# Kernel tuning notes

Hardware: AMD Instinct MI355X
Metric: run time of the kernel (lower is better)

## Reference

```python
import jax, jax.numpy as jnp
import numpy as np

INPUT_SIZE = 32
HIDDEN = 128
OUT_SIZE = 1
B, S = 256, 1200


def _gru_layer(x_seq, W_ih, W_hh, b_ih, b_hh):
    """PyTorch-convention GRU layer. x_seq: [B,S,D] -> [B,S,H].
    W_ih: [3H,D], W_hh: [3H,H], gate order (r,z,n)."""
    Bsz = x_seq.shape[0]
    H = W_hh.shape[1]
    # Precompute input projections for all timesteps (one big GEMM).
    gates_x = jnp.einsum('bsd,gd->bsg', x_seq, W_ih) + b_ih  # [B,S,3H]

    def step(h, gx):
        gh = h @ W_hh.T + b_hh                 # [B,3H]
        xr, xz, xn = jnp.split(gx, 3, axis=-1)
        hr, hz, hn = jnp.split(gh, 3, axis=-1)
        r = jax.nn.sigmoid(xr + hr)
        z = jax.nn.sigmoid(xz + hz)
        n = jnp.tanh(xn + r * hn)
        h_new = (1.0 - z) * n + z * h
        return h_new, h_new

    h0 = jnp.zeros((Bsz, H), x_seq.dtype)
    _, ys = jax.lax.scan(step, h0, jnp.swapaxes(gates_x, 0, 1))  # [S,B,H]
    return jnp.swapaxes(ys, 0, 1)


def setup_inputs() -> dict:
    key = jax.random.key(0)
    ks = jax.random.split(key, 12)
    s_in = 1.0 / np.sqrt(HIDDEN)  # PyTorch GRU init scale
    d = {
        'x': jax.random.normal(ks[0], (B, S, INPUT_SIZE), dtype=jnp.float32),
        'W_ih0': jax.random.uniform(ks[1], (3 * HIDDEN, INPUT_SIZE), jnp.float32, -s_in, s_in),
        'W_hh0': jax.random.uniform(ks[2], (3 * HIDDEN, HIDDEN), jnp.float32, -s_in, s_in),
        'b_ih0': jax.random.uniform(ks[3], (3 * HIDDEN,), jnp.float32, -s_in, s_in),
        'b_hh0': jax.random.uniform(ks[4], (3 * HIDDEN,), jnp.float32, -s_in, s_in),
        'W_ih1': jax.random.uniform(ks[5], (3 * HIDDEN, HIDDEN), jnp.float32, -s_in, s_in),
        'W_hh1': jax.random.uniform(ks[6], (3 * HIDDEN, HIDDEN), jnp.float32, -s_in, s_in),
        'b_ih1': jax.random.uniform(ks[7], (3 * HIDDEN,), jnp.float32, -s_in, s_in),
        'b_hh1': jax.random.uniform(ks[8], (3 * HIDDEN,), jnp.float32, -s_in, s_in),
        'W_lin': jax.random.uniform(ks[9], (OUT_SIZE, HIDDEN), jnp.float32, -s_in, s_in),
        'b_lin': jax.random.uniform(ks[10], (OUT_SIZE,), jnp.float32, -s_in, s_in),
    }
    return d


def reference(x, W_ih0, W_hh0, b_ih0, b_hh0, W_ih1, W_hh1, b_ih1, b_hh1, W_lin, b_lin):
    h1 = _gru_layer(x, W_ih0, W_hh0, b_ih0, b_hh0)   # [B,S,H]  (dropout inactive at eval)
    h2 = _gru_layer(h1, W_ih1, W_hh1, b_ih1, b_hh1)  # [B,S,H]
    out = jax.nn.relu(h2)
    out = jnp.einsum('bsh,oh->bso', out, W_lin) + b_lin  # [B,S,OUT_SIZE]
    return out.reshape(-1, 12)
```

## Files before the change

kernel.cpp:

```cpp
#include <hip/hip_runtime.h>
#include <hip/hip_bf16.h>


typedef _Float16 h2 __attribute__((ext_vector_type(2)));

#if __has_builtin(__builtin_amdgcn_fdot2)
__device__ __forceinline__ float dot2f(h2 a, h2 b, float c) {
  return __builtin_amdgcn_fdot2(a, b, c, false);
}
#else
__device__ __forceinline__ float dot2f(h2 a, h2 b, float c) {
  return c + (float)a[0] * (float)b[0] + (float)a[1] * (float)b[1];
}
#endif

__device__ __forceinline__ h2 pack2(float x, float y) {
  h2 r; r[0] = (_Float16)x; r[1] = (_Float16)y; return r;
}
__device__ __forceinline__ float sigm(float x) {
  return 1.0f / (1.0f + __expf(-x));
}
__device__ __forceinline__ float tanh_f(float x) {
  x = fminf(fmaxf(x, -15.f), 15.f);
  float e = __expf(2.f * x);
  return (e - 1.f) / (e + 1.f);
}
__device__ __forceinline__ float hsum(float4 v) { return (v.x + v.y) + (v.z + v.w); }

__device__ __forceinline__ void load_pack8(const float* p, h2* w) {
  float4 a = ((const float4*)p)[0], b = ((const float4*)p)[1];
  w[0] = pack2(a.x, a.y); w[1] = pack2(a.z, a.w);
  w[2] = pack2(b.x, b.y); w[3] = pack2(b.z, b.w);
}

#define SEQ 1200
#define HID 128
#define INSZ 32

#define DOT4Q(W, F, ACC)                                                \
  ACC = dot2f((W)[0], __builtin_bit_cast(h2, (F).x), ACC);              \
  ACC = dot2f((W)[1], __builtin_bit_cast(h2, (F).y), ACC);              \
  ACC = dot2f((W)[2], __builtin_bit_cast(h2, (F).z), ACC);              \
  ACC = dot2f((W)[3], __builtin_bit_cast(h2, (F).w), ACC);

#define DOT16Q(W, FA, FB, FC, FD, ACC)                                  \
  DOT4Q(&(W)[0],  FA, ACC) DOT4Q(&(W)[4],  FB, ACC)                     \
  DOT4Q(&(W)[8],  FC, ACC) DOT4Q(&(W)[12], FD, ACC)

__global__ __launch_bounds__(512, 2) void gru_fused(
    const float* __restrict__ x,
    const float* __restrict__ Wih0, const float* __restrict__ Whh0,
    const float* __restrict__ bih0, const float* __restrict__ bhh0,
    const float* __restrict__ Wih1, const float* __restrict__ Whh1,
    const float* __restrict__ bih1, const float* __restrict__ bhh1,
    const float* __restrict__ Wlin, const float* __restrict__ blin,
    float* __restrict__ out)
{
  const int tid = threadIdx.x;
  const int b   = blockIdx.x;
  const int q   = tid >> 2;
  const int ql  = tid & 3;

  __shared__ float G1p[4 * 512];
  __shared__ float G2p[4 * 512];
  __shared__ float  s0f[HID], s1f[HID];
  __shared__ float4 s0h4[16], s1h4[16];
  __shared__ float4 xh[2][4];
  __shared__ float  pbf[32];

  h2 wi0[3][4];
  h2 wh0[3][16];
  h2 wi1[3][16];
  h2 wh1[3][16];
#pragma unroll
  for (int rr = 0; rr < 3; ++rr) {
    const int row = rr * HID + q;
    load_pack8(Wih0 + (size_t)row * INSZ + ql * 8, wi0[rr]);
#pragma unroll
    for (int c = 0; c < 4; ++c) {
      load_pack8(Whh0 + (size_t)row * HID + ql * 32 + c * 8, &wh0[rr][c * 4]);
      load_pack8(Wih1 + (size_t)row * HID + ql * 32 + c * 8, &wi1[rr][c * 4]);
      load_pack8(Whh1 + (size_t)row * HID + ql * 32 + c * 8, &wh1[rr][c * 4]);
    }
  }

  float bA = 0.f, bB = 0.f, bC = 0.f, bD = 0.f, wl = 0.f;
  if (tid < 128) {
    bA = bih1[tid] + bhh1[tid];
    bB = bih1[HID + tid] + bhh1[HID + tid];
    bC = bih1[2 * HID + tid];
    bD = bhh1[2 * HID + tid];
    wl = Wlin[tid];
  } else if (tid < 256) {
    const int i = tid - 128;
    bA = bih0[i] + bhh0[i];
    bB = bih0[HID + i] + bhh0[HID + i];
    bC = bih0[2 * HID + i];
    bD = bhh0[2 * HID + i];
  }
  const float blv = blin[0];

  if (tid < HID) { s0f[tid] = 0.f; s1f[tid] = 0.f; }
  if (tid < 64) { ((float*)s0h4)[tid] = 0.f; ((float*)s1h4)[tid] = 0.f; }
  const float2* xsrc = (const float2*)x + (size_t)b * SEQ * (INSZ / 2);
  if (tid < 16) {
    float2 v = xsrc[tid];
    ((h2*)xh[0])[tid] = pack2(v.x, v.y);
  }
  __syncthreads();

  float* outp = out + (size_t)b * SEQ;

  for (int t = -1; t < SEQ; ++t) {
    {
      const int buf = (t + 1) & 1;
      const float4 xq = xh[buf][ql];
      const float4 sA = s0h4[ql * 4 + 0], sB = s0h4[ql * 4 + 1],
                   sC = s0h4[ql * 4 + 2], sD = s0h4[ql * 4 + 3];
      const float4 tA = s1h4[ql * 4 + 0], tB = s1h4[ql * 4 + 1],
                   tC = s1h4[ql * 4 + 2], tD = s1h4[ql * 4 + 3];
      float a0 = 0.f, a1 = 0.f, a2 = 0.f, a3 = 0.f;
      DOT4Q(wi0[0], xq, a0) DOT16Q(wh0[0], sA, sB, sC, sD, a0)
      DOT4Q(wi0[1], xq, a1) DOT16Q(wh0[1], sA, sB, sC, sD, a1)
      DOT4Q(wi0[2], xq, a2)
      DOT16Q(wh0[2], sA, sB, sC, sD, a3)
      float c0 = 0.f, c1 = 0.f, c2 = 0.f, c3 = 0.f;
      DOT16Q(wi1[0], sA, sB, sC, sD, c0) DOT16Q(wh1[0], tA, tB, tC, tD, c0)
      DOT16Q(wi1[1], sA, sB, sC, sD, c1) DOT16Q(wh1[1], tA, tB, tC, tD, c1)
      DOT16Q(wi1[2], sA, sB, sC, sD, c2)
      DOT16Q(wh1[2], tA, tB, tC, tD, c3)
      G1p[tid] = a0; G1p[512 + tid] = a1; G1p[1024 + tid] = a2; G1p[1536 + tid] = a3;
      G2p[tid] = c0; G2p[512 + tid] = c1; G2p[1024 + tid] = c2; G2p[1536 + tid] = c3;
    }
    float2 xn;
    if ((tid & ~15) == 256) {
      const int ti = (t + 2 < SEQ) ? t + 2 : SEQ - 1;
      xn = xsrc[(size_t)ti * 16 + (tid - 256)];
    }
    __syncthreads();

    if (tid < 128) {
      if (t >= 0) {
        const float4* G4 = (const float4*)G2p;
        float4 r4 = G4[tid], z4 = G4[128 + tid], x4 = G4[256 + tid], h4 = G4[384 + tid];
        float r = sigm(hsum(r4) + bA);
        float z = sigm(hsum(z4) + bB);
        float n = tanh_f(hsum(x4) + bC + r * (hsum(h4) + bD));
        float h = (1.f - z) * n + z * s1f[tid];
        s1f[tid] = h;
        ((_Float16*)s1h4)[tid] = (_Float16)h;
        float p = fmaxf(h, 0.f) * wl;
        p += __shfl_xor(p, 1, 64);
        p += __shfl_xor(p, 2, 64);
        p += __shfl_xor(p, 4, 64);
        if ((tid & 7) == 0) pbf[(t & 1) * 16 + (tid >> 3)] = p;
      }
    } else if (tid < 256) {
      const int i = tid - 128;
      const float4* G4 = (const float4*)G1p;
      float4 r4 = G4[i], z4 = G4[128 + i], x4 = G4[256 + i], h4 = G4[384 + i];
      float r = sigm(hsum(r4) + bA);
      float z = sigm(hsum(z4) + bB);
      float n = tanh_f(hsum(x4) + bC + r * (hsum(h4) + bD));
      float h = (1.f - z) * n + z * s0f[i];
      s0f[i] = h;
      ((_Float16*)s0h4)[i] = (_Float16)h;
    } else if (tid < 272) {
      ((h2*)xh[t & 1])[tid - 256] = pack2(xn.x, xn.y);
    } else if (tid == 320 && t >= 1) {
      const float4* p4 = (const float4*)(pbf + ((t - 1) & 1) * 16);
      outp[t - 1] = hsum(p4[0]) + hsum(p4[1]) + hsum(p4[2]) + hsum(p4[3]) + blv;
    }
    __syncthreads();
  }

  if (tid == 0) {
    const float4* p4 = (const float4*)(pbf + ((SEQ - 1) & 1) * 16);
    outp[SEQ - 1] = hsum(p4[0]) + hsum(p4[1]) + hsum(p4[2]) + hsum(p4[3]) + blv;
  }
}

extern "C" void kernel_launch(void* const* d_in, const int* in_sizes, int n_in,
                              void* d_out, int out_size, void* d_ws, size_t ws_size,
                              hipStream_t stream) {
  const float* x    = (const float*)d_in[0];
  const float* Wih0 = (const float*)d_in[1];
  const float* Whh0 = (const float*)d_in[2];
  const float* bih0 = (const float*)d_in[3];
  const float* bhh0 = (const float*)d_in[4];
  const float* Wih1 = (const float*)d_in[5];
  const float* Whh1 = (const float*)d_in[6];
  const float* bih1 = (const float*)d_in[7];
  const float* bhh1 = (const float*)d_in[8];
  const float* Wlin = (const float*)d_in[9];
  const float* blin = (const float*)d_in[10];
  float* outp = (float*)d_out;

  const int Bn = in_sizes[0] / (SEQ * INSZ);
  hipLaunchKernelGGL(gru_fused, dim3(Bn), dim3(512), 0, stream,
                     x, Wih0, Whh0, bih0, bhh0,
                     Wih1, Whh1, bih1, bhh1, Wlin, blin, outp);
}
```

Before: 1.354 ms.

## Split each gate-row dot product across eight threads with 1024-thread blocks

Doubles the block to 1024 threads so each gate row's dot products are split across 8 lanes instead of 4. Each thread now holds half as many packed fp16 weights in registers and does half the dot2 work per step, shortening the serial per-step critical path. In exchange, the gate-update threads must sum twice as many partials from shared memory, and barriers now span 16 waves. With 256 blocks, each CU likely holds only one block instead of possibly two.

```diff
diff --git a/kernel.cpp b/kernel.cpp
--- a/kernel.cpp
+++ b/kernel.cpp
@@ -43,11 +43,10 @@
   ACC = dot2f((W)[2], __builtin_bit_cast(h2, (F).z), ACC);              \
   ACC = dot2f((W)[3], __builtin_bit_cast(h2, (F).w), ACC);
 
-#define DOT16Q(W, FA, FB, FC, FD, ACC)                                  \
-  DOT4Q(&(W)[0],  FA, ACC) DOT4Q(&(W)[4],  FB, ACC)                     \
-  DOT4Q(&(W)[8],  FC, ACC) DOT4Q(&(W)[12], FD, ACC)
-
-__global__ __launch_bounds__(512, 2) void gru_fused(
+#define DOT8(W, FA, FB, ACC)                                            \
+  DOT4Q(&(W)[0], FA, ACC) DOT4Q(&(W)[4], FB, ACC)
+
+__global__ __launch_bounds__(1024) void gru_fused(
     const float* __restrict__ x,
     const float* __restrict__ Wih0, const float* __restrict__ Whh0,
     const float* __restrict__ bih0, const float* __restrict__ bhh0,
@@ -58,29 +57,30 @@
 {
   const int tid = threadIdx.x;
   const int b   = blockIdx.x;
-  const int q   = tid >> 2;
-  const int ql  = tid & 3;
-
-  __shared__ float G1p[4 * 512];
-  __shared__ float G2p[4 * 512];
+  const int oct = tid >> 3;
+  const int ko  = tid & 7;
+
+  __shared__ float G1p[4 * 1024];
+  __shared__ float G2p[4 * 1024];
   __shared__ float  s0f[HID], s1f[HID];
   __shared__ float4 s0h4[16], s1h4[16];
   __shared__ float4 xh[2][4];
   __shared__ float  pbf[32];
 
-  h2 wi0[3][4];
-  h2 wh0[3][16];
-  h2 wi1[3][16];
-  h2 wh1[3][16];
+  h2 wi0[3][2];
+  h2 wh0[3][8];
+  h2 wi1[3][8];
+  h2 wh1[3][8];
 #pragma unroll
   for (int rr = 0; rr < 3; ++rr) {
-    const int row = rr * HID + q;
-    load_pack8(Wih0 + (size_t)row * INSZ + ql * 8, wi0[rr]);
+    const int row = rr * HID + oct;
+    float4 v = *(const float4*)(Wih0 + (size_t)row * INSZ + ko * 4);
+    wi0[rr][0] = pack2(v.x, v.y); wi0[rr][1] = pack2(v.z, v.w);
 #pragma unroll
-    for (int c = 0; c < 4; ++c) {
-      load_pack8(Whh0 + (size_t)row * HID + ql * 32 + c * 8, &wh0[rr][c * 4]);
-      load_pack8(Wih1 + (size_t)row * HID + ql * 32 + c * 8, &wi1[rr][c * 4]);
-      load_pack8(Whh1 + (size_t)row * HID + ql * 32 + c * 8, &wh1[rr][c * 4]);
+    for (int c = 0; c < 2; ++c) {
+      load_pack8(Whh0 + (size_t)row * HID + ko * 16 + c * 8, &wh0[rr][c * 4]);
+      load_pack8(Wih1 + (size_t)row * HID + ko * 16 + c * 8, &wi1[rr][c * 4]);
+      load_pack8(Whh1 + (size_t)row * HID + ko * 16 + c * 8, &wh1[rr][c * 4]);
     }
   }
 
@@ -114,23 +114,25 @@
   for (int t = -1; t < SEQ; ++t) {
     {
       const int buf = (t + 1) & 1;
-      const float4 xq = xh[buf][ql];
-      const float4 sA = s0h4[ql * 4 + 0], sB = s0h4[ql * 4 + 1],
-                   sC = s0h4[ql * 4 + 2], sD = s0h4[ql * 4 + 3];
-      const float4 tA = s1h4[ql * 4 + 0], tB = s1h4[ql * 4 + 1],
-                   tC = s1h4[ql * 4 + 2], tD = s1h4[ql * 4 + 3];
+      const float2 xq = ((const float2*)xh[buf])[ko];
+      const h2 x0 = __builtin_bit_cast(h2, xq.x);
+      const h2 x1 = __builtin_bit_cast(h2, xq.y);
+      const float4 sA = s0h4[ko * 2], sB = s0h4[ko * 2 + 1];
+      const float4 tA = s1h4[ko * 2], tB = s1h4[ko * 2 + 1];
       float a0 = 0.f, a1 = 0.f, a2 = 0.f, a3 = 0.f;
-      DOT4Q(wi0[0], xq, a0) DOT16Q(wh0[0], sA, sB, sC, sD, a0)
-      DOT4Q(wi0[1], xq, a1) DOT16Q(wh0[1], sA, sB, sC, sD, a1)
-      DOT4Q(wi0[2], xq, a2)
-      DOT16Q(wh0[2], sA, sB, sC, sD, a3)
+      a0 = dot2f(wi0[0][0], x0, a0); a0 = dot2f(wi0[0][1], x1, a0);
+      DOT8(wh0[0], sA, sB, a0)
+      a1 = dot2f(wi0[1][0], x0, a1); a1 = dot2f(wi0[1][1], x1, a1);
+      DOT8(wh0[1], sA, sB, a1)
+      a2 = dot2f(wi0[2][0], x0, a2); a2 = dot2f(wi0[2][1], x1, a2);
+      DOT8(wh0[2], sA, sB, a3)
       float c0 = 0.f, c1 = 0.f, c2 = 0.f, c3 = 0.f;
-      DOT16Q(wi1[0], sA, sB, sC, sD, c0) DOT16Q(wh1[0], tA, tB, tC, tD, c0)
-      DOT16Q(wi1[1], sA, sB, sC, sD, c1) DOT16Q(wh1[1], tA, tB, tC, tD, c1)
-      DOT16Q(wi1[2], sA, sB, sC, sD, c2)
-      DOT16Q(wh1[2], tA, tB, tC, tD, c3)
-      G1p[tid] = a0; G1p[512 + tid] = a1; G1p[1024 + tid] = a2; G1p[1536 + tid] = a3;
-      G2p[tid] = c0; G2p[512 + tid] = c1; G2p[1024 + tid] = c2; G2p[1536 + tid] = c3;
+      DOT8(wi1[0], sA, sB, c0) DOT8(wh1[0], tA, tB, c0)
+      DOT8(wi1[1], sA, sB, c1) DOT8(wh1[1], tA, tB, c1)
+      DOT8(wi1[2], sA, sB, c2)
+      DOT8(wh1[2], tA, tB, c3)
+      G1p[tid] = a0; G1p[1024 + tid] = a1; G1p[2048 + tid] = a2; G1p[3072 + tid] = a3;
+      G2p[tid] = c0; G2p[1024 + tid] = c1; G2p[2048 + tid] = c2; G2p[3072 + tid] = c3;
     }
     float2 xn;
     if ((tid & ~15) == 256) {
@@ -142,10 +144,13 @@
     if (tid < 128) {
       if (t >= 0) {
         const float4* G4 = (const float4*)G2p;
-        float4 r4 = G4[tid], z4 = G4[128 + tid], x4 = G4[256 + tid], h4 = G4[384 + tid];
-        float r = sigm(hsum(r4) + bA);
-        float z = sigm(hsum(z4) + bB);
-        float n = tanh_f(hsum(x4) + bC + r * (hsum(h4) + bD));
+        float ra = hsum(G4[2 * tid])       + hsum(G4[2 * tid + 1]);
+        float za = hsum(G4[256 + 2 * tid]) + hsum(G4[257 + 2 * tid]);
+        float xa = hsum(G4[512 + 2 * tid]) + hsum(G4[513 + 2 * tid]);
+        float ha = hsum(G4[768 + 2 * tid]) + hsum(G4[769 + 2 * tid]);
+        float r = sigm(ra + bA);
+        float z = sigm(za + bB);
+        float n = tanh_f(xa + bC + r * (ha + bD));
         float h = (1.f - z) * n + z * s1f[tid];
         s1f[tid] = h;
         ((_Float16*)s1h4)[tid] = (_Float16)h;
@@ -158,10 +163,13 @@
     } else if (tid < 256) {
       const int i = tid - 128;
       const float4* G4 = (const float4*)G1p;
-      float4 r4 = G4[i], z4 = G4[128 + i], x4 = G4[256 + i], h4 = G4[384 + i];
-      float r = sigm(hsum(r4) + bA);
-      float z = sigm(hsum(z4) + bB);
-      float n = tanh_f(hsum(x4) + bC + r * (hsum(h4) + bD));
+      float ra = hsum(G4[2 * i])       + hsum(G4[2 * i + 1]);
+      float za = hsum(G4[256 + 2 * i]) + hsum(G4[257 + 2 * i]);
+      float xa = hsum(G4[512 + 2 * i]) + hsum(G4[513 + 2 * i]);
+      float ha = hsum(G4[768 + 2 * i]) + hsum(G4[769 + 2 * i]);
+      float r = sigm(ra + bA);
+      float z = sigm(za + bB);
+      float n = tanh_f(xa + bC + r * (ha + bD));
       float h = (1.f - z) * n + z * s0f[i];
       s0f[i] = h;
       ((_Float16*)s0h4)[i] = (_Float16)h;
@@ -197,7 +205,7 @@
   float* outp = (float*)d_out;
 
   const int Bn = in_sizes[0] / (SEQ * INSZ);
-  hipLaunchKernelGGL(gru_fused, dim3(Bn), dim3(512), 0, stream,
+  hipLaunchKernelGGL(gru_fused, dim3(Bn), dim3(1024), 0, stream,
                      x, Wih0, Whh0, bih0, bhh0,
                      Wih1, Whh1, bih1, bhh1, Wlin, blin, outp);
 }
```

After: 1.447 ms. 6.9% more time.

## Compute GRU gate matvecs with MFMA 16x16x32 f16 instead of fdot2

Applied to the files above, without the earlier changes.

Replaces the per-thread fdot2 matrix-vector products with MFMA instructions. Weights stay in registers as f16x8 A-fragments and the hidden state is broadcast as the B operand, so only column 0 of each 16x16 output is useful. Each wave covers 32 r/z rows and 16 n rows and writes the gate pre-activations to shared memory from lanes with lr==0. This removes the four-way partial-sum reduction and cuts instruction count per step, but wastes most of the MFMA output width and drops launch bounds to one block per CU.

```diff
diff --git a/kernel.cpp b/kernel.cpp
--- a/kernel.cpp
+++ b/kernel.cpp
@@ -2,21 +2,13 @@
 #include <hip/hip_bf16.h>
 
 
-typedef _Float16 h2 __attribute__((ext_vector_type(2)));
-
-#if __has_builtin(__builtin_amdgcn_fdot2)
-__device__ __forceinline__ float dot2f(h2 a, h2 b, float c) {
-  return __builtin_amdgcn_fdot2(a, b, c, false);
-}
-#else
-__device__ __forceinline__ float dot2f(h2 a, h2 b, float c) {
-  return c + (float)a[0] * (float)b[0] + (float)a[1] * (float)b[1];
-}
-#endif
-
-__device__ __forceinline__ h2 pack2(float x, float y) {
-  h2 r; r[0] = (_Float16)x; r[1] = (_Float16)y; return r;
-}
+typedef _Float16 f16x8 __attribute__((ext_vector_type(8)));
+typedef float f32x4 __attribute__((ext_vector_type(4)));
+
+#define SEQ 1200
+#define HID 128
+#define INSZ 32
+
 __device__ __forceinline__ float sigm(float x) {
   return 1.0f / (1.0f + __expf(-x));
 }
@@ -25,29 +17,18 @@
   float e = __expf(2.f * x);
   return (e - 1.f) / (e + 1.f);
 }
-__device__ __forceinline__ float hsum(float4 v) { return (v.x + v.y) + (v.z + v.w); }
-
-__device__ __forceinline__ void load_pack8(const float* p, h2* w) {
-  float4 a = ((const float4*)p)[0], b = ((const float4*)p)[1];
-  w[0] = pack2(a.x, a.y); w[1] = pack2(a.z, a.w);
-  w[2] = pack2(b.x, b.y); w[3] = pack2(b.z, b.w);
-}
-
-#define SEQ 1200
-#define HID 128
-#define INSZ 32
-
-#define DOT4Q(W, F, ACC)                                                \
-  ACC = dot2f((W)[0], __builtin_bit_cast(h2, (F).x), ACC);              \
-  ACC = dot2f((W)[1], __builtin_bit_cast(h2, (F).y), ACC);              \
-  ACC = dot2f((W)[2], __builtin_bit_cast(h2, (F).z), ACC);              \
-  ACC = dot2f((W)[3], __builtin_bit_cast(h2, (F).w), ACC);
-
-#define DOT16Q(W, FA, FB, FC, FD, ACC)                                  \
-  DOT4Q(&(W)[0],  FA, ACC) DOT4Q(&(W)[4],  FB, ACC)                     \
-  DOT4Q(&(W)[8],  FC, ACC) DOT4Q(&(W)[12], FD, ACC)
-
-__global__ __launch_bounds__(512, 2) void gru_fused(
+
+__device__ __forceinline__ f16x8 loadA(const float* p) {
+  float4 u = ((const float4*)p)[0], v = ((const float4*)p)[1];
+  f16x8 r;
+  r[0] = (_Float16)u.x; r[1] = (_Float16)u.y; r[2] = (_Float16)u.z; r[3] = (_Float16)u.w;
+  r[4] = (_Float16)v.x; r[5] = (_Float16)v.y; r[6] = (_Float16)v.z; r[7] = (_Float16)v.w;
+  return r;
+}
+
+#define MFMA(A, B, C) __builtin_amdgcn_mfma_f32_16x16x32_f16((A), (B), (C), 0, 0, 0)
+
+__global__ __launch_bounds__(512, 1) void gru_fused(
     const float* __restrict__ x,
     const float* __restrict__ Wih0, const float* __restrict__ Whh0,
     const float* __restrict__ bih0, const float* __restrict__ bhh0,
@@ -56,31 +37,42 @@
     const float* __restrict__ Wlin, const float* __restrict__ blin,
     float* __restrict__ out)
 {
-  const int tid = threadIdx.x;
-  const int b   = blockIdx.x;
-  const int q   = tid >> 2;
-  const int ql  = tid & 3;
-
-  __shared__ float G1p[4 * 512];
-  __shared__ float G2p[4 * 512];
-  __shared__ float  s0f[HID], s1f[HID];
-  __shared__ float4 s0h4[16], s1h4[16];
-  __shared__ float4 xh[2][4];
-  __shared__ float  pbf[32];
-
-  h2 wi0[3][4];
-  h2 wh0[3][16];
-  h2 wi1[3][16];
-  h2 wh1[3][16];
+  const int tid  = threadIdx.x;
+  const int b    = blockIdx.x;
+  const int wid  = tid >> 6;
+  const int lane = tid & 63;
+  const int lr   = lane & 15;
+  const int lg   = lane >> 4;
+
+  __shared__ float G1x[384], G1h[384];
+  __shared__ float G2x[384], G2h[384];
+  __shared__ float s0f[HID], s1f[HID];
+  __shared__ __align__(16) _Float16 s0h[HID], s1h[HID];
+  __shared__ __align__(16) _Float16 xh[2][INSZ];
+  __shared__ float pbf[32];
+
+  const int RZ0 = wid * 32, RZ1 = wid * 32 + 16, NR = 256 + wid * 16;
+
+  f16x8 Ax0, Ax1, AxN;
+  f16x8 Ah0[3][4], Ai1[3][4], Ah1w[3][4];
+  {
+    const int r0 = RZ0 + lr, r1 = RZ1 + lr, rn = NR + lr;
+    const int kb = lg * 8;
+    Ax0 = loadA(Wih0 + (size_t)r0 * INSZ + kb);
+    Ax1 = loadA(Wih0 + (size_t)r1 * INSZ + kb);
+    AxN = loadA(Wih0 + (size_t)rn * INSZ + kb);
 #pragma unroll
-  for (int rr = 0; rr < 3; ++rr) {
-    const int row = rr * HID + q;
-    load_pack8(Wih0 + (size_t)row * INSZ + ql * 8, wi0[rr]);
-#pragma unroll
-    for (int c = 0; c < 4; ++c) {
-      load_pack8(Whh0 + (size_t)row * HID + ql * 32 + c * 8, &wh0[rr][c * 4]);
-      load_pack8(Wih1 + (size_t)row * HID + ql * 32 + c * 8, &wi1[rr][c * 4]);
-      load_pack8(Whh1 + (size_t)row * HID + ql * 32 + c * 8, &wh1[rr][c * 4]);
+    for (int kt = 0; kt < 4; ++kt) {
+      const int ko = kt * 32 + kb;
+      Ah0[0][kt]  = loadA(Whh0 + (size_t)r0 * HID + ko);
+      Ah0[1][kt]  = loadA(Whh0 + (size_t)r1 * HID + ko);
+      Ah0[2][kt]  = loadA(Whh0 + (size_t)rn * HID + ko);
+      Ai1[0][kt]  = loadA(Wih1 + (size_t)r0 * HID + ko);
+      Ai1[1][kt]  = loadA(Wih1 + (size_t)r1 * HID + ko);
+      Ai1[2][kt]  = loadA(Wih1 + (size_t)rn * HID + ko);
+      Ah1w[0][kt] = loadA(Whh1 + (size_t)r0 * HID + ko);
+      Ah1w[1][kt] = loadA(Whh1 + (size_t)r1 * HID + ko);
+      Ah1w[2][kt] = loadA(Whh1 + (size_t)rn * HID + ko);
     }
   }
 
@@ -100,12 +92,14 @@
   }
   const float blv = blin[0];
 
-  if (tid < HID) { s0f[tid] = 0.f; s1f[tid] = 0.f; }
-  if (tid < 64) { ((float*)s0h4)[tid] = 0.f; ((float*)s1h4)[tid] = 0.f; }
+  if (tid < HID) {
+    s0f[tid] = 0.f; s1f[tid] = 0.f;
+    s0h[tid] = (_Float16)0.f; s1h[tid] = (_Float16)0.f;
+  }
   const float2* xsrc = (const float2*)x + (size_t)b * SEQ * (INSZ / 2);
   if (tid < 16) {
     float2 v = xsrc[tid];
-    ((h2*)xh[0])[tid] = pack2(v.x, v.y);
+    xh[0][2 * tid] = (_Float16)v.x; xh[0][2 * tid + 1] = (_Float16)v.y;
   }
   __syncthreads();
 
@@ -113,24 +107,43 @@
 
   for (int t = -1; t < SEQ; ++t) {
     {
-      const int buf = (t + 1) & 1;
-      const float4 xq = xh[buf][ql];
-      const float4 sA = s0h4[ql * 4 + 0], sB = s0h4[ql * 4 + 1],
-                   sC = s0h4[ql * 4 + 2], sD = s0h4[ql * 4 + 3];
-      const float4 tA = s1h4[ql * 4 + 0], tB = s1h4[ql * 4 + 1],
-                   tC = s1h4[ql * 4 + 2], tD = s1h4[ql * 4 + 3];
-      float a0 = 0.f, a1 = 0.f, a2 = 0.f, a3 = 0.f;
-      DOT4Q(wi0[0], xq, a0) DOT16Q(wh0[0], sA, sB, sC, sD, a0)
-      DOT4Q(wi0[1], xq, a1) DOT16Q(wh0[1], sA, sB, sC, sD, a1)
-      DOT4Q(wi0[2], xq, a2)
-      DOT16Q(wh0[2], sA, sB, sC, sD, a3)
-      float c0 = 0.f, c1 = 0.f, c2 = 0.f, c3 = 0.f;
-      DOT16Q(wi1[0], sA, sB, sC, sD, c0) DOT16Q(wh1[0], tA, tB, tC, tD, c0)
-      DOT16Q(wi1[1], sA, sB, sC, sD, c1) DOT16Q(wh1[1], tA, tB, tC, tD, c1)
-      DOT16Q(wi1[2], sA, sB, sC, sD, c2)
-      DOT16Q(wh1[2], tA, tB, tC, tD, c3)
-      G1p[tid] = a0; G1p[512 + tid] = a1; G1p[1024 + tid] = a2; G1p[1536 + tid] = a3;
-      G2p[tid] = c0; G2p[512 + tid] = c1; G2p[1024 + tid] = c2; G2p[1536 + tid] = c3;
+      f16x8 Bh1[4], Bh2[4], Bx;
+#pragma unroll
+      for (int kt = 0; kt < 4; ++kt) {
+        Bh1[kt] = *(const f16x8*)(s0h + kt * 32 + lg * 8);
+        Bh2[kt] = *(const f16x8*)(s1h + kt * 32 + lg * 8);
+      }
+      Bx = *(const f16x8*)(xh[(t + 1) & 1] + lg * 8);
+
+      const f32x4 Z = {0.f, 0.f, 0.f, 0.f};
+      f32x4 a0x = MFMA(Ax0, Bx, Z);
+      f32x4 a1x = MFMA(Ax1, Bx, Z);
+      f32x4 anx = MFMA(AxN, Bx, Z);
+      f32x4 a0h = Z, a1h = Z, anh = Z;
+      f32x4 c0x = Z, c1x = Z, cnx = Z, c0h = Z, c1h = Z, cnh = Z;
+#pragma unroll
+      for (int kt = 0; kt < 4; ++kt) {
+        a0h = MFMA(Ah0[0][kt],  Bh1[kt], a0h);
+        a1h = MFMA(Ah0[1][kt],  Bh1[kt], a1h);
+        anh = MFMA(Ah0[2][kt],  Bh1[kt], anh);
+        c0x = MFMA(Ai1[0][kt],  Bh1[kt], c0x);
+        c1x = MFMA(Ai1[1][kt],  Bh1[kt], c1x);
+        cnx = MFMA(Ai1[2][kt],  Bh1[kt], cnx);
+        c0h = MFMA(Ah1w[0][kt], Bh2[kt], c0h);
+        c1h = MFMA(Ah1w[1][kt], Bh2[kt], c1h);
+        cnh = MFMA(Ah1w[2][kt], Bh2[kt], cnh);
+      }
+      if (lr == 0) {
+        const int ro = lg * 4;
+        *(f32x4*)(G1x + RZ0 + ro) = a0x; *(f32x4*)(G1x + RZ1 + ro) = a1x;
+        *(f32x4*)(G1x + NR  + ro) = anx;
+        *(f32x4*)(G1h + RZ0 + ro) = a0h; *(f32x4*)(G1h + RZ1 + ro) = a1h;
+        *(f32x4*)(G1h + NR  + ro) = anh;
+        *(f32x4*)(G2x + RZ0 + ro) = c0x; *(f32x4*)(G2x + RZ1 + ro) = c1x;
+        *(f32x4*)(G2x + NR  + ro) = cnx;
+        *(f32x4*)(G2h + RZ0 + ro) = c0h; *(f32x4*)(G2h + RZ1 + ro) = c1h;
+        *(f32x4*)(G2h + NR  + ro) = cnh;
+      }
     }
     float2 xn;
     if ((tid & ~15) == 256) {
@@ -141,14 +154,12 @@
 
     if (tid < 128) {
       if (t >= 0) {
-        const float4* G4 = (const float4*)G2p;
-        float4 r4 = G4[tid], z4 = G4[128 + tid], x4 = G4[256 + tid], h4 = G4[384 + tid];
-        float r = sigm(hsum(r4) + bA);
-        float z = sigm(hsum(z4) + bB);
-        float n = tanh_f(hsum(x4) + bC + r * (hsum(h4) + bD));
+        float r = sigm(G2x[tid] + G2h[tid] + bA);
+        float z = sigm(G2x[HID + tid] + G2h[HID + tid] + bB);
+        float n = tanh_f(G2x[2 * HID + tid] + bC + r * (G2h[2 * HID + tid] + bD));
         float h = (1.f - z) * n + z * s1f[tid];
         s1f[tid] = h;
-        ((_Float16*)s1h4)[tid] = (_Float16)h;
+        s1h[tid] = (_Float16)h;
         float p = fmaxf(h, 0.f) * wl;
         p += __shfl_xor(p, 1, 64);
         p += __shfl_xor(p, 2, 64);
@@ -157,26 +168,29 @@
       }
     } else if (tid < 256) {
       const int i = tid - 128;
-      const float4* G4 = (const float4*)G1p;
-      float4 r4 = G4[i], z4 = G4[128 + i], x4 = G4[256 + i], h4 = G4[384 + i];
-      float r = sigm(hsum(r4) + bA);
-      float z = sigm(hsum(z4) + bB);
-      float n = tanh_f(hsum(x4) + bC + r * (hsum(h4) + bD));
+      float r = sigm(G1x[i] + G1h[i] + bA);
+      float z = sigm(G1x[HID + i] + G1h[HID + i] + bB);
+      float n = tanh_f(G1x[2 * HID + i] + bC + r * (G1h[2 * HID + i] + bD));
       float h = (1.f - z) * n + z * s0f[i];
       s0f[i] = h;
-      ((_Float16*)s0h4)[i] = (_Float16)h;
+      s0h[i] = (_Float16)h;
     } else if (tid < 272) {
-      ((h2*)xh[t & 1])[tid - 256] = pack2(xn.x, xn.y);
+      const int i = tid - 256;
+      xh[t & 1][2 * i] = (_Float16)xn.x; xh[t & 1][2 * i + 1] = (_Float16)xn.y;
     } else if (tid == 320 && t >= 1) {
       const float4* p4 = (const float4*)(pbf + ((t - 1) & 1) * 16);
-      outp[t - 1] = hsum(p4[0]) + hsum(p4[1]) + hsum(p4[2]) + hsum(p4[3]) + blv;
+      float4 u = p4[0], v = p4[1], w = p4[2], s = p4[3];
+      outp[t - 1] = (u.x + u.y + u.z + u.w) + (v.x + v.y + v.z + v.w) +
+                    (w.x + w.y + w.z + w.w) + (s.x + s.y + s.z + s.w) + blv;
     }
     __syncthreads();
   }
 
   if (tid == 0) {
     const float4* p4 = (const float4*)(pbf + ((SEQ - 1) & 1) * 16);
-    outp[SEQ - 1] = hsum(p4[0]) + hsum(p4[1]) + hsum(p4[2]) + hsum(p4[3]) + blv;
+    float4 u = p4[0], v = p4[1], w = p4[2], s = p4[3];
+    outp[SEQ - 1] = (u.x + u.y + u.z + u.w) + (v.x + v.y + v.z + v.w) +
+                    (w.x + w.y + w.z + w.w) + (s.x + s.y + s.z + s.w) + blv;
   }
 }
 
```

New measurement: 1.836 ms. +35.6%, slower.
